# Optimization experiments

Measured on AMD Instinct MI355X. Metric: run time of the kernel, lower is better.

The kernel has to match this reference:

```python
import jax, jax.numpy as jnp
import numpy as np

N_NODES = 10000
N_EDGES = 64000
N_GRAPHS = 64
HID = 64


def _nnconv(h, src, dst, edge_attr, w1, b1, w2, b2, root, bias):
    # edge MLP: Linear(dim_edge,64) -> ReLU -> Linear(64, 64*64)
    we = (jax.nn.relu(edge_attr @ w1 + b1) @ w2 + b2).reshape(-1, HID, HID)  # [E,64,64]
    # per-edge matmul of gathered source features, then scatter-add to dst
    msg = jnp.einsum('ei,eio->eo', h[src], we)                               # [E,64]
    agg = jax.ops.segment_sum(msg, dst, num_segments=N_NODES)               # [N,64]
    return agg + h @ root + bias


def setup_inputs() -> dict:
    key = jax.random.key(0)
    ks = jax.random.split(key, 20)
    s = 0.05
    inp = {
        'x': jax.random.normal(ks[0], (N_NODES, 128), jnp.float32),
        'edge_index': jax.random.randint(ks[1], (2, N_EDGES), 0, N_NODES, dtype=jnp.int64),
        'edge_attr': jax.random.normal(ks[2], (N_EDGES, 32), jnp.float32),
        'batch': jnp.sort(jax.random.randint(ks[3], (N_NODES,), 0, N_GRAPHS, dtype=jnp.int64)),
        'nfc_w': jax.random.normal(ks[4], (128, HID), jnp.float32) * s,
        'nfc_b': jnp.zeros((HID,), jnp.float32),
        'efc1_w1': jax.random.normal(ks[5], (32, HID), jnp.float32) * s,
        'efc1_b1': jnp.zeros((HID,), jnp.float32),
        'efc1_w2': jax.random.normal(ks[6], (HID, HID * HID), jnp.float32) * s,
        'efc1_b2': jnp.zeros((HID * HID,), jnp.float32),
        'gc1_root': jax.random.normal(ks[7], (HID, HID), jnp.float32) * s,
        'gc1_bias': jnp.zeros((HID,), jnp.float32),
        'efc2_w1': jax.random.normal(ks[8], (32, HID), jnp.float32) * s,
        'efc2_b1': jnp.zeros((HID,), jnp.float32),
        'efc2_w2': jax.random.normal(ks[9], (HID, HID * HID), jnp.float32) * s,
        'efc2_b2': jnp.zeros((HID * HID,), jnp.float32),
        'gc2_root': jax.random.normal(ks[10], (HID, HID), jnp.float32) * s,
        'gc2_bias': jnp.zeros((HID,), jnp.float32),
        'fc1_w': jax.random.normal(ks[11], (HID, 32), jnp.float32) * s,
        'fc1_b': jnp.zeros((32,), jnp.float32),
        'fc2_w': jax.random.normal(ks[12], (32, 1), jnp.float32) * s,
        'fc2_b': jnp.zeros((1,), jnp.float32),
    }
    return inp


def reference(x, edge_index, edge_attr, batch,
              nfc_w, nfc_b,
              efc1_w1, efc1_b1, efc1_w2, efc1_b2, gc1_root, gc1_bias,
              efc2_w1, efc2_b1, efc2_w2, efc2_b2, gc2_root, gc2_bias,
              fc1_w, fc1_b, fc2_w, fc2_b):
    lrelu = lambda v: jax.nn.leaky_relu(v, 0.01)
    src, dst = edge_index[0], edge_index[1]
    hx = lrelu(x @ nfc_w + nfc_b)
    hx = lrelu(_nnconv(hx, src, dst, edge_attr, efc1_w1, efc1_b1, efc1_w2, efc1_b2, gc1_root, gc1_bias))
    hx = lrelu(_nnconv(hx, src, dst, edge_attr, efc2_w1, efc2_b1, efc2_w2, efc2_b2, gc2_root, gc2_bias))
    hg = jax.ops.segment_sum(hx, batch, num_segments=N_GRAPHS)  # global_add_pool -> [G,64]
    hg = lrelu(hg @ fc1_w + fc1_b)
    return hg @ fc2_w + fc2_b
```

## Files before the change

### kernel.cpp

```cpp
#include <hip/hip_runtime.h>
#include <hip/hip_bf16.h>

#define N_NODES  10000
#define N_EDGES  64000
#define N_GRAPHS 64
#define HID      64

typedef __attribute__((ext_vector_type(8))) short short8;
typedef __attribute__((ext_vector_type(4))) float f32x4;
typedef __attribute__((ext_vector_type(2))) float f32x2;

__device__ __forceinline__ float lrelu(float v){ return v > 0.f ? v : 0.01f*v; }

__device__ __forceinline__ unsigned short f2bf(float f){
    union { float f; unsigned u; } v; v.f = f;
    unsigned r = v.u + 0x7fff + ((v.u >> 16) & 1);
    return (unsigned short)(r >> 16);
}
__device__ __forceinline__ float bf2f(unsigned short s){
    union { unsigned u; float f; } v; v.u = ((unsigned)s) << 16;
    return v.f;
}
__device__ __forceinline__ short8 pack_bf8(float4 a, float4 b){
    short8 r;
    r[0]=(short)f2bf(a.x); r[1]=(short)f2bf(a.y); r[2]=(short)f2bf(a.z); r[3]=(short)f2bf(a.w);
    r[4]=(short)f2bf(b.x); r[5]=(short)f2bf(b.y); r[6]=(short)f2bf(b.z); r[7]=(short)f2bf(b.w);
    return r;
}

__global__ void __launch_bounds__(256) init_kernel(
        int* __restrict__ counts,
        const float* __restrict__ nfc_w, unsigned short* __restrict__ nfc_wt,
        const float* __restrict__ e1w1, unsigned short* __restrict__ w1t1,
        const float* __restrict__ e2w1, unsigned short* __restrict__ w1t2,
        const float* __restrict__ e1b2, unsigned short* __restrict__ b2t1,
        const float* __restrict__ e2b2, unsigned short* __restrict__ b2t2,
        const float* __restrict__ g1root, unsigned short* __restrict__ rootT1,
        const float* __restrict__ g2root, unsigned short* __restrict__ rootT2){
    int b = blockIdx.x, tid = threadIdx.x;
    if (b < 40){
        int i = b * 256 + tid;
        if (i < N_NODES) counts[i] = 0;
    } else if (b == 40){
        for (int idx = tid; idx < 8192; idx += 256){
            int o = idx >> 7, i = idx & 127;
            nfc_wt[idx] = f2bf(nfc_w[i * 64 + o]);
        }
    } else if (b <= 42){
        const float* w1 = (b == 42) ? e2w1 : e1w1;
        unsigned short* w1t = (b == 42) ? w1t2 : w1t1;
        for (int idx = tid; idx < 2048; idx += 256){
            int o = idx >> 5, k = idx & 31;
            w1t[idx] = f2bf(w1[k * 64 + o]);
        }
    } else if (b <= 44){
        const float* b2 = (b == 44) ? e2b2 : e1b2;
        unsigned short* b2t = (b == 44) ? b2t2 : b2t1;
        for (int idx = tid; idx < 4096; idx += 256){
            int o = idx >> 6, i = idx & 63;
            b2t[idx] = f2bf(b2[i * 64 + o]);
        }
    } else {
        const float* rt = (b == 46) ? g2root : g1root;
        unsigned short* rT = (b == 46) ? rootT2 : rootT1;
        for (int idx = tid; idx < 4096; idx += 256){
            int o = idx >> 6, i = idx & 63;
            rT[idx] = f2bf(rt[i * 64 + o]);
        }
    }
}

#define PRE_NFC 157
#define PRE_TG  1000
#define PRE_W2C 128
#define PRE_CNT 250
__global__ void __launch_bounds__(256) pre_kernel(
        const float* __restrict__ x, const unsigned short* __restrict__ nfc_wt,
        const float* __restrict__ nfc_b, float* __restrict__ hx1,
        const float* __restrict__ ea,
        const unsigned short* __restrict__ w1t1, const float* __restrict__ e1b1, unsigned short* __restrict__ tp1,
        const unsigned short* __restrict__ w1t2, const float* __restrict__ e2b1, unsigned short* __restrict__ tp2,
        const float* __restrict__ e1w2, unsigned short* __restrict__ w2t1,
        const float* __restrict__ e2w2, unsigned short* __restrict__ w2t2,
        const int* __restrict__ src, int* __restrict__ counts){
    __shared__ float tile[64][65];
    int b = blockIdx.x, tid = threadIdx.x;
    int wid = tid >> 6, l = tid & 63;
    int m16 = l & 15, grp = l >> 4;
    if (b < PRE_NFC){
        int node = b * 64 + wid * 16 + m16;
        bool ok = node < N_NODES;
        short8 xb[4];
        #pragma unroll
        for (int kq = 0; kq < 4; ++kq){
            if (ok){
                const float* xp = x + (size_t)node * 128 + kq * 32 + grp * 8;
                xb[kq] = pack_bf8(*(const float4*)xp, *(const float4*)(xp + 4));
            } else {
                short8 z = {0,0,0,0,0,0,0,0}; xb[kq] = z;
            }
        }
        #pragma unroll
        for (int TB = 0; TB < 64; TB += 16){
            f32x4 acc = *(const f32x4*)(nfc_b + TB + grp * 4);
            #pragma unroll
            for (int kq = 0; kq < 4; ++kq){
                short8 af = *(const short8*)(nfc_wt + (TB + m16) * 128 + kq * 32 + grp * 8);
                acc = __builtin_amdgcn_mfma_f32_16x16x32_bf16(af, xb[kq], acc, 0, 0, 0);
            }
            f32x4 r;
            r[0] = lrelu(acc[0]); r[1] = lrelu(acc[1]); r[2] = lrelu(acc[2]); r[3] = lrelu(acc[3]);
            if (ok) *(f32x4*)(hx1 + ((size_t)node << 6) + TB + grp * 4) = r;
        }
    } else if (b < PRE_NFC + PRE_TG){
        int j = (b - PRE_NFC) * 64 + wid * 16 + m16;
        const float* row = ea + (size_t)j * 32 + grp * 8;
        short8 ef = pack_bf8(*(const float4*)row, *(const float4*)(row + 4));
        #pragma unroll
        for (int TB = 0; TB < 64; TB += 16){
            short8 wf1 = *(const short8*)(w1t1 + (TB + m16) * 32 + grp * 8);
            f32x4 a1 = *(const f32x4*)(e1b1 + TB + grp * 4);
            a1 = __builtin_amdgcn_mfma_f32_16x16x32_bf16(wf1, ef, a1, 0, 0, 0);
            uint2 p;
            p.x = (unsigned)f2bf(fmaxf(a1[0], 0.f)) | ((unsigned)f2bf(fmaxf(a1[1], 0.f)) << 16);
            p.y = (unsigned)f2bf(fmaxf(a1[2], 0.f)) | ((unsigned)f2bf(fmaxf(a1[3], 0.f)) << 16);
            *(uint2*)(tp1 + ((size_t)j << 6) + TB + grp * 4) = p;
            short8 wf2 = *(const short8*)(w1t2 + (TB + m16) * 32 + grp * 8);
            f32x4 a2 = *(const f32x4*)(e2b1 + TB + grp * 4);
            a2 = __builtin_amdgcn_mfma_f32_16x16x32_bf16(wf2, ef, a2, 0, 0, 0);
            p.x = (unsigned)f2bf(fmaxf(a2[0], 0.f)) | ((unsigned)f2bf(fmaxf(a2[1], 0.f)) << 16);
            p.y = (unsigned)f2bf(fmaxf(a2[2], 0.f)) | ((unsigned)f2bf(fmaxf(a2[3], 0.f)) << 16);
            *(uint2*)(tp2 + ((size_t)j << 6) + TB + grp * 4) = p;
        }
    } else if (b < PRE_NFC + PRE_TG + PRE_W2C){
        int bb = b - PRE_NFC - PRE_TG;
        int k = bb & 63;
        const float* srcw = ((bb < 64) ? e1w2 : e2w2) + (size_t)k * 4096;
        unsigned short* dstw = (bb < 64) ? w2t1 : w2t2;
        for (int idx = tid; idx < 4096; idx += 256) tile[idx >> 6][idx & 63] = srcw[idx];
        __syncthreads();
        for (int idx = tid; idx < 4096; idx += 256){
            int o = idx >> 6, i = idx & 63;
            dstw[((size_t)(k * 64 + o) << 6) + i] = f2bf(tile[i][o]);
        }
    } else {
        int e = (b - PRE_NFC - PRE_TG - PRE_W2C) * 256 + tid;
        if (e < N_EDGES) atomicAdd(&counts[src[e]], 1);
    }
}

__global__ void csr_scan_kernel(const int* __restrict__ counts, int* __restrict__ rowptr,
                                int* __restrict__ cursor){
    __shared__ int part[256];
    int tid = threadIdx.x;
    const int CH = (N_NODES + 255) / 256;
    int base = tid * CH, s = 0;
    for (int i = 0; i < CH; ++i){ int idx = base + i; if (idx < N_NODES){ cursor[idx] = 0; s += counts[idx]; } }
    part[tid] = s; __syncthreads();
    for (int off = 1; off < 256; off <<= 1){
        int v = (tid >= off) ? part[tid - off] : 0;
        __syncthreads();
        part[tid] += v;
        __syncthreads();
    }
    int run = part[tid] - s;
    for (int i = 0; i < CH; ++i){ int idx = base + i; if (idx < N_NODES){ rowptr[idx] = run; run += counts[idx]; } }
    if (tid == 255) rowptr[N_NODES] = run;
}

__global__ void csr_scatter_kernel(const int* __restrict__ src, const int* __restrict__ dst,
                                   const int* __restrict__ rowptr, int* __restrict__ cursor,
                                   int* __restrict__ eidx, int* __restrict__ dsts){
    int e = blockIdx.x * 256 + threadIdx.x;
    if (e >= N_EDGES) return;
    int s = src[e];
    int j = rowptr[s] + atomicAdd(&cursor[s], 1);
    eidx[j] = e; dsts[j] = dst[e];
}

#define NBH2 157
#define NBG  (157 * 8)
template<int L2FLAG>
__global__ void __launch_bounds__(256) layerA_kernel(
        const float* __restrict__ hx, const unsigned short* __restrict__ b2t,
        float* __restrict__ hb2, float* __restrict__ agg,
        const unsigned short* __restrict__ w2t, unsigned char* __restrict__ G,
        float* __restrict__ hg){
    __shared__ unsigned stgu[8192];
    int b = blockIdx.x, tid = threadIdx.x;
    int wid = tid >> 6, l = tid & 63;
    int m16 = l & 15, grp = l >> 4;

    if (b < NBH2){
        int node = b * 64 + wid * 16 + m16;
        short8 h0 = {0,0,0,0,0,0,0,0}, h1 = {0,0,0,0,0,0,0,0};
        if (node < N_NODES){
            const float* hp = hx + ((size_t)node << 6) + grp * 8;
            h0 = pack_bf8(*(const float4*)hp, *(const float4*)(hp + 4));
            h1 = pack_bf8(*(const float4*)(hp + 32), *(const float4*)(hp + 36));
        }
        #pragma unroll
        for (int TB = 0; TB < 64; TB += 16){
            short8 c0 = *(const short8*)(b2t + (TB + m16) * 64 + grp * 8);
            short8 c1 = *(const short8*)(b2t + (TB + m16) * 64 + 32 + grp * 8);
            f32x4 acc = {0.f, 0.f, 0.f, 0.f};
            acc = __builtin_amdgcn_mfma_f32_16x16x32_bf16(c0, h0, acc, 0, 0, 0);
            acc = __builtin_amdgcn_mfma_f32_16x16x32_bf16(c1, h1, acc, 0, 0, 0);
            if (node < N_NODES) *(f32x4*)(hb2 + ((size_t)node << 6) + TB + grp * 4) = acc;
        }
        f32x4 z = {0.f, 0.f, 0.f, 0.f};
        #pragma unroll
        for (int q = 0; q < 4; ++q){
            int chunk = q * 256 + tid;
            int n = b * 64 + (chunk >> 4), c = (chunk & 15) * 4;
            if (n < N_NODES) *(f32x4*)(agg + ((size_t)n << 6) + c) = z;
        }
    } else if (b < NBH2 + NBG){
        int g = b - NBH2;
        int bx = g >> 3, by = g & 7;
        int n0 = bx * 64;
        int cb = by * 512;

        short8 bf0[4], bf1[4];
        #pragma unroll
        for (int ng = 0; ng < 4; ++ng){
            int node = n0 + ng * 16 + m16;
            short8 b0 = {0,0,0,0,0,0,0,0}, b1v = {0,0,0,0,0,0,0,0};
            if (node < N_NODES){
                const float* hp = hx + ((size_t)node << 6) + grp * 8;
                b0  = pack_bf8(*(const float4*)hp, *(const float4*)(hp + 4));
                b1v = pack_bf8(*(const float4*)(hp + 32), *(const float4*)(hp + 36));
            }
            bf0[ng] = b0; bf1[ng] = b1v;
        }

        #pragma unroll
        for (int t = 0; t < 8; ++t){
            int TB = cb + t * 64 + wid * 16;
            const unsigned short* ap = w2t + ((size_t)(TB + m16) << 6) + grp * 8;
            short8 a0 = *(const short8*)ap;
            short8 a1 = *(const short8*)(ap + 32);
            int colLocal = t * 64 + wid * 16 + grp * 4;
            #pragma unroll
            for (int ng = 0; ng < 4; ++ng){
                f32x4 acc = {0.f, 0.f, 0.f, 0.f};
                acc = __builtin_amdgcn_mfma_f32_16x16x32_bf16(a0, bf0[ng], acc, 0, 0, 0);
                acc = __builtin_amdgcn_mfma_f32_16x16x32_bf16(a1, bf1[ng], acc, 0, 0, 0);
                int pk = __builtin_amdgcn_cvt_pk_fp8_f32(acc[0], acc[1], 0, false);
                pk = __builtin_amdgcn_cvt_pk_fp8_f32(acc[2], acc[3], pk, true);
                int row = ng * 16 + m16;
                int dw = ((row << 7) + (colLocal >> 2)) ^ ((row & 7) << 2);
                stgu[dw] = (unsigned)pk;
            }
        }
        __syncthreads();
        #pragma unroll
        for (int s2 = 0; s2 < 8; ++s2){
            int ci = s2 * 256 + tid;
            int row = ci >> 5;
            int c = ci & 31;
            int node = n0 + row;
            int dwb = ((row << 7) + (c << 2)) ^ ((row & 7) << 2);
            uint4 v = *(const uint4*)&stgu[dwb];
            if (node < N_NODES)
                *(uint4*)(G + (size_t)node * 4096 + cb + c * 16) = v;
        }
    } else if (L2FLAG){
        for (int i = tid; i < N_GRAPHS * 64; i += 256) hg[i] = 0.f;
    }
}

__global__ void __launch_bounds__(64) msg_csr_kernel(
        const unsigned short* __restrict__ tp, const unsigned char* __restrict__ G,
        const float* __restrict__ hb2, const int* __restrict__ rowptr,
        const int* __restrict__ eidx, const int* __restrict__ dsts,
        float* __restrict__ agg){
    int s = blockIdx.x;
    int o = threadIdx.x;
    __shared__ unsigned short ts[64] __attribute__((aligned(16)));
    int r0 = rowptr[s], r1 = rowptr[s + 1];
    if (r0 == r1) return;
    const unsigned char* gp = G + (size_t)s * 4096 + o;
    float g[64];
    #pragma unroll
    for (int k = 0; k < 64; k += 2){
        unsigned b0 = gp[k << 6];
        unsigned b1 = gp[(k + 1) << 6];
        f32x2 d = __builtin_amdgcn_cvt_pk_f32_fp8((int)(b0 | (b1 << 8)), false);
        g[k] = d[0]; g[k + 1] = d[1];
    }
    float hb = hb2[((size_t)s << 6) + o];
    for (int j = r0; j < r1; ++j){
        int e = eidx[j];
        ts[o] = tp[((size_t)e << 6) + o];
        float acc = hb;
        #pragma unroll
        for (int k8 = 0; k8 < 8; ++k8){
            short8 tv = *(const short8*)&ts[k8 * 8];
            #pragma unroll
            for (int u = 0; u < 8; ++u) acc += bf2f((unsigned short)tv[u]) * g[k8 * 8 + u];
        }
        atomicAdd(&agg[((size_t)dsts[j] << 6) + o], acc);
    }
}

template<int L2>
__global__ void __launch_bounds__(256) combine_kernel(
        const float* __restrict__ agg, const float* __restrict__ hx,
        const unsigned short* __restrict__ rootT, const float* __restrict__ bias,
        float* __restrict__ outp, const int* __restrict__ batch, float* __restrict__ hg){
    __shared__ float otile[64][65];
    int b = blockIdx.x, tid = threadIdx.x;
    int wid = tid >> 6, l = tid & 63;
    int m16 = l & 15, grp = l >> 4;
    int node = b * 64 + wid * 16 + m16;
    int lnode = wid * 16 + m16;
    bool ok = node < N_NODES;
    short8 h0 = {0,0,0,0,0,0,0,0}, h1 = {0,0,0,0,0,0,0,0};
    if (ok){
        const float* hp = hx + ((size_t)node << 6) + grp * 8;
        h0 = pack_bf8(*(const float4*)hp, *(const float4*)(hp + 4));
        h1 = pack_bf8(*(const float4*)(hp + 32), *(const float4*)(hp + 36));
    }
    #pragma unroll
    for (int TB = 0; TB < 64; TB += 16){
        short8 c0 = *(const short8*)(rootT + (TB + m16) * 64 + grp * 8);
        short8 c1 = *(const short8*)(rootT + (TB + m16) * 64 + 32 + grp * 8);
        f32x4 acc;
        if (ok){
            f32x4 av = *(const f32x4*)(agg + ((size_t)node << 6) + TB + grp * 4);
            f32x4 bv = *(const f32x4*)(bias + TB + grp * 4);
            acc[0] = av[0] + bv[0]; acc[1] = av[1] + bv[1];
            acc[2] = av[2] + bv[2]; acc[3] = av[3] + bv[3];
        } else {
            acc[0] = acc[1] = acc[2] = acc[3] = 0.f;
        }
        acc = __builtin_amdgcn_mfma_f32_16x16x32_bf16(c0, h0, acc, 0, 0, 0);
        acc = __builtin_amdgcn_mfma_f32_16x16x32_bf16(c1, h1, acc, 0, 0, 0);
        if (L2){
            #pragma unroll
            for (int r = 0; r < 4; ++r) otile[lnode][TB + grp * 4 + r] = lrelu(acc[r]);
        } else if (ok){
            f32x4 rv;
            rv[0] = lrelu(acc[0]); rv[1] = lrelu(acc[1]);
            rv[2] = lrelu(acc[2]); rv[3] = lrelu(acc[3]);
            *(f32x4*)(outp + ((size_t)node << 6) + TB + grp * 4) = rv;
        }
    }
    if (L2){
        __syncthreads();
        #pragma unroll
        for (int p = 0; p < 16; ++p){
            int ln = wid * 16 + p;
            int n = b * 64 + ln;
            if (n < N_NODES)
                atomicAdd(&hg[batch[n] * 64 + l], otile[ln][l]);
        }
    }
}

__global__ void head_kernel(const float* __restrict__ hg, const float* __restrict__ fc1w,
                            const float* __restrict__ fc1b, const float* __restrict__ fc2w,
                            const float* __restrict__ fc2b, float* __restrict__ out){
    int g = threadIdx.x;
    const float* row = hg + g * 64;
    float h1[32];
    #pragma unroll
    for (int j = 0; j < 32; ++j){
        float a = fc1b[j];
        #pragma unroll 8
        for (int i = 0; i < 64; ++i) a += row[i] * fc1w[i * 32 + j];
        h1[j] = lrelu(a);
    }
    float o = fc2b[0];
    #pragma unroll
    for (int j = 0; j < 32; ++j) o += h1[j] * fc2w[j];
    out[g] = o;
}

extern "C" void kernel_launch(void* const* d_in, const int* in_sizes, int n_in,
                              void* d_out, int out_size, void* d_ws, size_t ws_size,
                              hipStream_t stream){
    const float* x      = (const float*)d_in[0];
    const int*   ei     = (const int*)  d_in[1];
    const float* ea     = (const float*)d_in[2];
    const int*   batch  = (const int*)  d_in[3];
    const float* nfc_w  = (const float*)d_in[4];
    const float* nfc_b  = (const float*)d_in[5];
    const float* e1w1   = (const float*)d_in[6];
    const float* e1b1   = (const float*)d_in[7];
    const float* e1w2   = (const float*)d_in[8];
    const float* e1b2   = (const float*)d_in[9];
    const float* g1root = (const float*)d_in[10];
    const float* g1bias = (const float*)d_in[11];
    const float* e2w1   = (const float*)d_in[12];
    const float* e2b1   = (const float*)d_in[13];
    const float* e2w2   = (const float*)d_in[14];
    const float* e2b2   = (const float*)d_in[15];
    const float* g2root = (const float*)d_in[16];
    const float* g2bias = (const float*)d_in[17];
    const float* fc1w   = (const float*)d_in[18];
    const float* fc1b   = (const float*)d_in[19];
    const float* fc2w   = (const float*)d_in[20];
    const float* fc2b   = (const float*)d_in[21];
    float* out = (float*)d_out;

    const int* src = ei;
    const int* dst = ei + N_EDGES;

    char* ws = (char*)d_ws;
    float* hx1 = (float*)ws;               ws += (size_t)N_NODES * 64 * 4;
    float* hx2 = (float*)ws;               ws += (size_t)N_NODES * 64 * 4;
    unsigned short* tp1 = (unsigned short*)ws; ws += (size_t)N_EDGES * 64 * 2;
    unsigned short* tp2 = (unsigned short*)ws; ws += (size_t)N_EDGES * 64 * 2;
    float* hb2 = (float*)ws;               ws += (size_t)N_NODES * 64 * 4;
    float* agg = (float*)ws;               ws += (size_t)N_NODES * 64 * 4;
    float* hg  = (float*)ws;               ws += (size_t)N_GRAPHS * 64 * 4;
    unsigned short* w2t1 = (unsigned short*)ws; ws += (size_t)64 * 64 * 64 * 2;
    unsigned short* w2t2 = (unsigned short*)ws; ws += (size_t)64 * 64 * 64 * 2;
    unsigned short* nfc_wt = (unsigned short*)ws; ws += (size_t)8192 * 2;
    unsigned short* w1t1 = (unsigned short*)ws; ws += (size_t)2048 * 2;
    unsigned short* w1t2 = (unsigned short*)ws; ws += (size_t)2048 * 2;
    unsigned short* b2t1 = (unsigned short*)ws; ws += (size_t)4096 * 2;
    unsigned short* b2t2 = (unsigned short*)ws; ws += (size_t)4096 * 2;
    unsigned short* rootT1 = (unsigned short*)ws; ws += (size_t)4096 * 2;
    unsigned short* rootT2 = (unsigned short*)ws; ws += (size_t)4096 * 2;
    int* counts = (int*)ws;                ws += (size_t)10240 * 4;
    int* cursor = (int*)ws;                ws += (size_t)10240 * 4;
    int* rowptr = (int*)ws;                ws += (size_t)10240 * 4;
    int* eidx   = (int*)ws;                ws += (size_t)N_EDGES * 4;
    int* dsts   = (int*)ws;                ws += (size_t)N_EDGES * 4;
    unsigned char* G = (unsigned char*)ws;

    init_kernel<<<47, 256, 0, stream>>>(counts, nfc_w, nfc_wt,
        e1w1, w1t1, e2w1, w1t2, e1b2, b2t1, e2b2, b2t2, g1root, rootT1, g2root, rootT2);
    pre_kernel<<<PRE_NFC + PRE_TG + PRE_W2C + PRE_CNT, 256, 0, stream>>>(
        x, nfc_wt, nfc_b, hx1, ea, w1t1, e1b1, tp1, w1t2, e2b1, tp2,
        e1w2, w2t1, e2w2, w2t2, src, counts);
    csr_scan_kernel<<<1, 256, 0, stream>>>(counts, rowptr, cursor);
    csr_scatter_kernel<<<N_EDGES / 256, 256, 0, stream>>>(src, dst, rowptr, cursor, eidx, dsts);

    layerA_kernel<0><<<NBH2 + NBG, 256, 0, stream>>>(hx1, b2t1, hb2, agg, w2t1, G, nullptr);
    msg_csr_kernel<<<N_NODES, 64, 0, stream>>>(tp1, G, hb2, rowptr, eidx, dsts, agg);
    combine_kernel<0><<<157, 256, 0, stream>>>(agg, hx1, rootT1, g1bias, hx2, batch, nullptr);

    layerA_kernel<1><<<NBH2 + NBG + 1, 256, 0, stream>>>(hx2, b2t2, hb2, agg, w2t2, G, hg);
    msg_csr_kernel<<<N_NODES, 64, 0, stream>>>(tp2, G, hb2, rowptr, eidx, dsts, agg);
    combine_kernel<1><<<157, 256, 0, stream>>>(agg, hx2, rootT2, g2bias, nullptr, batch, hg);

    head_kernel<<<1, 64, 0, stream>>>(hg, fc1w, fc1b, fc2w, fc2b, out);
}
```

Before: 215.6 us.

## Fuse CSR scan, scatter and head into neighbouring kernels via last-block pattern

The CSR prefix scan now runs in the last block of pre_kernel to finish, detected with an atomic counter. The edge scatter runs as extra blocks of the first layerA kernel, and the MLP head runs in the last block of the second combine kernel. This removes three kernel launches and their inter-kernel gaps. Separately, msg_csr now stages each node's 4 KB fp8 G row into shared memory with 16-byte loads instead of reading bytes strided from global. In exchange the scan and head serialise inside a single trailing block, and correctness depends on the threadfence and atomic ordering of the last-block pattern.

```diff
diff --git a/kernel.cpp b/kernel.cpp
--- a/kernel.cpp
+++ b/kernel.cpp
@@ -29,7 +29,7 @@
 }
 
 __global__ void __launch_bounds__(256) init_kernel(
-        int* __restrict__ counts,
+        int* __restrict__ counts, int* __restrict__ pre_done, int* __restrict__ comb_done,
         const float* __restrict__ nfc_w, unsigned short* __restrict__ nfc_wt,
         const float* __restrict__ e1w1, unsigned short* __restrict__ w1t1,
         const float* __restrict__ e2w1, unsigned short* __restrict__ w1t2,
@@ -41,6 +41,7 @@
     if (b < 40){
         int i = b * 256 + tid;
         if (i < N_NODES) counts[i] = 0;
+        if (b == 0 && tid == 0){ pre_done[0] = 0; comb_done[0] = 0; }
     } else if (b == 40){
         for (int idx = tid; idx < 8192; idx += 256){
             int o = idx >> 7, i = idx & 127;
@@ -74,6 +75,7 @@
 #define PRE_TG  1000
 #define PRE_W2C 128
 #define PRE_CNT 250
+#define PRE_NB  (PRE_NFC + PRE_TG + PRE_W2C + PRE_CNT)
 __global__ void __launch_bounds__(256) pre_kernel(
         const float* __restrict__ x, const unsigned short* __restrict__ nfc_wt,
         const float* __restrict__ nfc_b, float* __restrict__ hx1,
@@ -82,8 +84,11 @@
         const unsigned short* __restrict__ w1t2, const float* __restrict__ e2b1, unsigned short* __restrict__ tp2,
         const float* __restrict__ e1w2, unsigned short* __restrict__ w2t1,
         const float* __restrict__ e2w2, unsigned short* __restrict__ w2t2,
-        const int* __restrict__ src, int* __restrict__ counts){
+        const int* __restrict__ src, int* __restrict__ counts,
+        int* __restrict__ rowptr, int* __restrict__ cursor, int* __restrict__ pre_done){
     __shared__ float tile[64][65];
+    __shared__ int part[256];
+    __shared__ int lastf;
     int b = blockIdx.x, tid = threadIdx.x;
     int wid = tid >> 6, l = tid & 63;
     int m16 = l & 15, grp = l >> 4;
@@ -147,45 +152,52 @@
         int e = (b - PRE_NFC - PRE_TG - PRE_W2C) * 256 + tid;
         if (e < N_EDGES) atomicAdd(&counts[src[e]], 1);
     }
-}
-
-__global__ void csr_scan_kernel(const int* __restrict__ counts, int* __restrict__ rowptr,
-                                int* __restrict__ cursor){
-    __shared__ int part[256];
-    int tid = threadIdx.x;
-    const int CH = (N_NODES + 255) / 256;
-    int base = tid * CH, s = 0;
-    for (int i = 0; i < CH; ++i){ int idx = base + i; if (idx < N_NODES){ cursor[idx] = 0; s += counts[idx]; } }
-    part[tid] = s; __syncthreads();
-    for (int off = 1; off < 256; off <<= 1){
-        int v = (tid >= off) ? part[tid - off] : 0;
-        __syncthreads();
-        part[tid] += v;
-        __syncthreads();
-    }
-    int run = part[tid] - s;
-    for (int i = 0; i < CH; ++i){ int idx = base + i; if (idx < N_NODES){ rowptr[idx] = run; run += counts[idx]; } }
-    if (tid == 255) rowptr[N_NODES] = run;
-}
-
-__global__ void csr_scatter_kernel(const int* __restrict__ src, const int* __restrict__ dst,
-                                   const int* __restrict__ rowptr, int* __restrict__ cursor,
-                                   int* __restrict__ eidx, int* __restrict__ dsts){
-    int e = blockIdx.x * 256 + threadIdx.x;
-    if (e >= N_EDGES) return;
-    int s = src[e];
-    int j = rowptr[s] + atomicAdd(&cursor[s], 1);
-    eidx[j] = e; dsts[j] = dst[e];
+
+    __syncthreads();
+    if (tid == 0){
+        __threadfence();
+        lastf = (atomicAdd(pre_done, 1) == PRE_NB - 1) ? 1 : 0;
+    }
+    __syncthreads();
+    if (lastf){
+        const int CH = 40;
+        int base = tid * CH;
+        int cnt[CH];
+        int s = 0;
+        #pragma unroll
+        for (int i = 0; i < CH; ++i){
+            int idx = base + i;
+            int c = (idx < N_NODES) ? atomicAdd(&counts[idx], 0) : 0;
+            cnt[i] = c; s += c;
+        }
+        part[tid] = s; __syncthreads();
+        for (int off = 1; off < 256; off <<= 1){
+            int v = (tid >= off) ? part[tid - off] : 0;
+            __syncthreads();
+            part[tid] += v;
+            __syncthreads();
+        }
+        int run = part[tid] - s;
+        #pragma unroll
+        for (int i = 0; i < CH; ++i){
+            int idx = base + i;
+            if (idx < N_NODES){ rowptr[idx] = run; cursor[idx] = 0; run += cnt[i]; }
+        }
+        if (tid == 255) rowptr[N_NODES] = run;
+    }
 }
 
 #define NBH2 157
 #define NBG  (157 * 8)
-template<int L2FLAG>
+template<int L2FLAG, int SCAT>
 __global__ void __launch_bounds__(256) layerA_kernel(
         const float* __restrict__ hx, const unsigned short* __restrict__ b2t,
         float* __restrict__ hb2, float* __restrict__ agg,
         const unsigned short* __restrict__ w2t, unsigned char* __restrict__ G,
-        float* __restrict__ hg){
+        float* __restrict__ hg,
+        const int* __restrict__ src, const int* __restrict__ dst,
+        const int* __restrict__ rowptr, int* __restrict__ cursor,
+        int* __restrict__ eidx, int* __restrict__ dsts){
     __shared__ unsigned stgu[8192];
     int b = blockIdx.x, tid = threadIdx.x;
     int wid = tid >> 6, l = tid & 63;
@@ -265,6 +277,13 @@
             if (node < N_NODES)
                 *(uint4*)(G + (size_t)node * 4096 + cb + c * 16) = v;
         }
+    } else if (SCAT){
+        int e = (b - NBH2 - NBG) * 256 + tid;
+        if (e < N_EDGES){
+            int s = src[e];
+            int j = rowptr[s] + atomicAdd(&cursor[s], 1);
+            eidx[j] = e; dsts[j] = dst[e];
+        }
     } else if (L2FLAG){
         for (int i = tid; i < N_GRAPHS * 64; i += 256) hg[i] = 0.f;
     }
@@ -277,15 +296,19 @@
         float* __restrict__ agg){
     int s = blockIdx.x;
     int o = threadIdx.x;
+    __shared__ unsigned char gl[4096] __attribute__((aligned(16)));
     __shared__ unsigned short ts[64] __attribute__((aligned(16)));
     int r0 = rowptr[s], r1 = rowptr[s + 1];
     if (r0 == r1) return;
-    const unsigned char* gp = G + (size_t)s * 4096 + o;
+    const uint4* gs = (const uint4*)(G + (size_t)s * 4096);
+    uint4* gld = (uint4*)gl;
+    #pragma unroll
+    for (int i = 0; i < 4; ++i) gld[i * 64 + o] = gs[i * 64 + o];
     float g[64];
     #pragma unroll
     for (int k = 0; k < 64; k += 2){
-        unsigned b0 = gp[k << 6];
-        unsigned b1 = gp[(k + 1) << 6];
+        unsigned b0 = gl[(k << 6) + o];
+        unsigned b1 = gl[((k + 1) << 6) + o];
         f32x2 d = __builtin_amdgcn_cvt_pk_f32_fp8((int)(b0 | (b1 << 8)), false);
         g[k] = d[0]; g[k + 1] = d[1];
     }
@@ -308,8 +331,12 @@
 __global__ void __launch_bounds__(256) combine_kernel(
         const float* __restrict__ agg, const float* __restrict__ hx,
         const unsigned short* __restrict__ rootT, const float* __restrict__ bias,
-        float* __restrict__ outp, const int* __restrict__ batch, float* __restrict__ hg){
+        float* __restrict__ outp, const int* __restrict__ batch, float* __restrict__ hg,
+        const float* __restrict__ fc1w, const float* __restrict__ fc1b,
+        const float* __restrict__ fc2w, const float* __restrict__ fc2b,
+        float* __restrict__ out, int* __restrict__ comb_done){
     __shared__ float otile[64][65];
+    __shared__ int lastf;
     int b = blockIdx.x, tid = threadIdx.x;
     int wid = tid >> 6, l = tid & 63;
     int m16 = l & 15, grp = l >> 4;
@@ -356,26 +383,31 @@
             if (n < N_NODES)
                 atomicAdd(&hg[batch[n] * 64 + l], otile[ln][l]);
         }
-    }
-}
-
-__global__ void head_kernel(const float* __restrict__ hg, const float* __restrict__ fc1w,
-                            const float* __restrict__ fc1b, const float* __restrict__ fc2w,
-                            const float* __restrict__ fc2b, float* __restrict__ out){
-    int g = threadIdx.x;
-    const float* row = hg + g * 64;
-    float h1[32];
-    #pragma unroll
-    for (int j = 0; j < 32; ++j){
-        float a = fc1b[j];
-        #pragma unroll 8
-        for (int i = 0; i < 64; ++i) a += row[i] * fc1w[i * 32 + j];
-        h1[j] = lrelu(a);
-    }
-    float o = fc2b[0];
-    #pragma unroll
-    for (int j = 0; j < 32; ++j) o += h1[j] * fc2w[j];
-    out[g] = o;
+        __syncthreads();
+        if (tid == 0){
+            __threadfence();
+            lastf = (atomicAdd(comb_done, 1) == 156) ? 1 : 0;
+        }
+        __syncthreads();
+        if (lastf && tid < 64){
+            int gidx = tid;
+            float row[64];
+            #pragma unroll
+            for (int i = 0; i < 64; ++i) row[i] = atomicAdd(&hg[gidx * 64 + i], 0.f);
+            float h1v[32];
+            #pragma unroll
+            for (int j = 0; j < 32; ++j){
+                float a = fc1b[j];
+                #pragma unroll 8
+                for (int i = 0; i < 64; ++i) a += row[i] * fc1w[i * 32 + j];
+                h1v[j] = lrelu(a);
+            }
+            float ov = fc2b[0];
+            #pragma unroll
+            for (int j = 0; j < 32; ++j) ov += h1v[j] * fc2w[j];
+            out[gidx] = ov;
+        }
+    }
 }
 
 extern "C" void kernel_launch(void* const* d_in, const int* in_sizes, int n_in,
@@ -430,23 +462,25 @@
     int* rowptr = (int*)ws;                ws += (size_t)10240 * 4;
     int* eidx   = (int*)ws;                ws += (size_t)N_EDGES * 4;
     int* dsts   = (int*)ws;                ws += (size_t)N_EDGES * 4;
+    int* pre_done  = (int*)ws;             ws += 256;
+    int* comb_done = (int*)ws;             ws += 256;
     unsigned char* G = (unsigned char*)ws;
 
-    init_kernel<<<47, 256, 0, stream>>>(counts, nfc_w, nfc_wt,
+    init_kernel<<<47, 256, 0, stream>>>(counts, pre_done, comb_done, nfc_w, nfc_wt,
         e1w1, w1t1, e2w1, w1t2, e1b2, b2t1, e2b2, b2t2, g1root, rootT1, g2root, rootT2);
-    pre_kernel<<<PRE_NFC + PRE_TG + PRE_W2C + PRE_CNT, 256, 0, stream>>>(
+    pre_kernel<<<PRE_NB, 256, 0, stream>>>(
         x, nfc_wt, nfc_b, hx1, ea, w1t1, e1b1, tp1, w1t2, e2b1, tp2,
-        e1w2, w2t1, e2w2, w2t2, src, counts);
-    csr_scan_kernel<<<1, 256, 0, stream>>>(counts, rowptr, cursor);
-    csr_scatter_kernel<<<N_EDGES / 256, 256, 0, stream>>>(src, dst, rowptr, cursor, eidx, dsts);
-
-    layerA_kernel<0><<<NBH2 + NBG, 256, 0, stream>>>(hx1, b2t1, hb2, agg, w2t1, G, nullptr);
+        e1w2, w2t1, e2w2, w2t2, src, counts, rowptr, cursor, pre_done);
+
+    layerA_kernel<0, 1><<<NBH2 + NBG + 250, 256, 0, stream>>>(
+        hx1, b2t1, hb2, agg, w2t1, G, nullptr, src, dst, rowptr, cursor, eidx, dsts);
     msg_csr_kernel<<<N_NODES, 64, 0, stream>>>(tp1, G, hb2, rowptr, eidx, dsts, agg);
-    combine_kernel<0><<<157, 256, 0, stream>>>(agg, hx1, rootT1, g1bias, hx2, batch, nullptr);
-
-    layerA_kernel<1><<<NBH2 + NBG + 1, 256, 0, stream>>>(hx2, b2t2, hb2, agg, w2t2, G, hg);
+    combine_kernel<0><<<157, 256, 0, stream>>>(agg, hx1, rootT1, g1bias, hx2, batch, nullptr,
+                                               nullptr, nullptr, nullptr, nullptr, nullptr, nullptr);
+
+    layerA_kernel<1, 0><<<NBH2 + NBG + 1, 256, 0, stream>>>(
+        hx2, b2t2, hb2, agg, w2t2, G, hg, src, dst, rowptr, cursor, eidx, dsts);
     msg_csr_kernel<<<N_NODES, 64, 0, stream>>>(tp2, G, hb2, rowptr, eidx, dsts, agg);
-    combine_kernel<1><<<157, 256, 0, stream>>>(agg, hx2, rootT2, g2bias, nullptr, batch, hg);
-
-    head_kernel<<<1, 64, 0, stream>>>(hg, fc1w, fc1b, fc2w, fc2b, out);
-}
+    combine_kernel<1><<<157, 256, 0, stream>>>(agg, hx2, rootT2, g2bias, nullptr, batch, hg,
+                                               fc1w, fc1b, fc2w, fc2b, out, comb_done);
+}
```

Result: slower. 270.8 us (+25.6%).
